# Kernel tuning notes

Measured on AMD Instinct MI355X. Metric: run time of the kernel, lower is better.

The kernel has to match this reference:

```python
import jax, jax.numpy as jnp
import numpy as np

BS, N_AGENTS, SA_DIM, HID = 2048, 64, 128, 256


def setup_inputs() -> dict:
    key = jax.random.key(0)
    ks = jax.random.split(key, 16)
    s = lambda fan_in: 1.0 / np.sqrt(fan_in)
    u = lambda k, shp, b: jax.random.uniform(k, shp, jnp.float32, -b, b)
    return {
        "x": jax.random.normal(ks[0], (BS, N_AGENTS, SA_DIM), jnp.float32),
        # encoder: Linear(sa, hid) -> Linear(hid, hid)
        "enc_w1": u(ks[1], (SA_DIM, HID), s(SA_DIM)),
        "enc_b1": u(ks[2], (HID,), s(SA_DIM)),
        "enc_w2": u(ks[3], (HID, HID), s(HID)),
        "enc_b2": u(ks[4], (HID,), s(HID)),
        # attention 'general' linear_in (no bias)
        "attn_w": u(ks[5], (HID, HID), s(HID)),
        # gc1: Linear(sa, hid); nn_gc1: Linear(sa, hid)
        "gc1_w": u(ks[6], (SA_DIM, HID), s(SA_DIM)),
        "gc1_b": u(ks[7], (HID,), s(SA_DIM)),
        "nn1_w": u(ks[8], (SA_DIM, HID), s(SA_DIM)),
        "nn1_b": u(ks[9], (HID,), s(SA_DIM)),
        # gc2: Linear(hid, hid); nn_gc2: Linear(hid, hid)
        "gc2_w": u(ks[10], (HID, HID), s(HID)),
        "gc2_b": u(ks[11], (HID,), s(HID)),
        "nn2_w": u(ks[12], (HID, HID), s(HID)),
        "nn2_b": u(ks[13], (HID,), s(HID)),
        "n_agents": N_AGENTS,
    }


def reference(x, enc_w1, enc_b1, enc_w2, enc_b2, attn_w,
              gc1_w, gc1_b, nn1_w, nn1_b, gc2_w, gc2_b, nn2_w, nn2_b,
              n_agents):
    relu = jax.nn.relu
    inv_n = 1.0 / n_agents
    # encoder MLP: relu(relu(x W1 + b1) W2 + b2)  -> [bs, n, hid]
    emb = relu(relu(x @ enc_w1 + enc_b1) @ enc_w2 + enc_b2)
    # general attention: softmax((emb W_a) emb^T) over last axis -> [bs, n, n]
    scores = jnp.einsum('bnd,bmd->bnm', emb @ attn_w, emb)
    attn = jax.nn.softmax(scores, axis=-1)
    # gc1: adj @ Linear(x); residual relu branch; normalize by n_agents
    feat = relu(jnp.einsum('bnm,bmh->bnh', attn, x @ gc1_w + gc1_b))
    feat = (feat + relu(x @ nn1_w + nn1_b)) * inv_n
    # gc2 on feat
    out = relu(jnp.einsum('bnm,bmh->bnh', attn, feat @ gc2_w + gc2_b))
    out = (out + relu(feat @ nn2_w + nn2_b)) * inv_n
    return out, attn
```

## Files before the change

### kernel.cpp

```cpp
#include <hip/hip_runtime.h>

typedef _Float16 half8 __attribute__((ext_vector_type(8)));
typedef _Float16 half4_t __attribute__((ext_vector_type(4)));
typedef float f32x4 __attribute__((ext_vector_type(4)));

#define NBATCH 2048
#define NA 64
#define SA 128
#define HID 256

#define OFF_R0 0
#define OFF_ATT 16384
#define SMEM_BYTES 40960

#define W_ENC1 0
#define W_ENC2 (W_ENC1 + 128 * 256)
#define W_ATTN (W_ENC2 + 256 * 256)
#define W_GC1 (W_ATTN + 256 * 256)
#define W_NN1 (W_GC1 + 128 * 256)
#define W_GC2 (W_NN1 + 128 * 256)
#define W_NN2 (W_GC2 + 256 * 256)

#define MFMA(a, b, cacc) __builtin_amdgcn_mfma_f32_16x16x32_f16((a), (b), (cacc), 0, 0, 0)

#define BAR()                                            \
  do {                                                   \
    asm volatile("s_waitcnt lgkmcnt(0)" ::: "memory");   \
    __builtin_amdgcn_s_barrier();                        \
  } while (0)

__global__ void pack_all(const float* __restrict__ e1, const float* __restrict__ e2,
                         const float* __restrict__ aw, const float* __restrict__ g1,
                         const float* __restrict__ n1, const float* __restrict__ g2,
                         const float* __restrict__ n2, _Float16* __restrict__ dst) {
  int b = (int)blockIdx.x;
  const float* src;
  int off;
  if (b < 16) { src = e1; off = W_ENC1; }
  else if (b < 48) { src = e2; off = W_ENC2; b -= 16; }
  else if (b < 80) { src = aw; off = W_ATTN; b -= 48; }
  else if (b < 96) { src = g1; off = W_GC1; b -= 80; }
  else if (b < 112) { src = n1; off = W_NN1; b -= 96; }
  else if (b < 144) { src = g2; off = W_GC2; b -= 112; }
  else { src = n2; off = W_NN2; b -= 144; }
  int t = b * 256 + (int)threadIdx.x;
  int lane = t & 63, frag = t >> 6;
  int nt = frag & 15, kt = frag >> 4;
  int g = lane >> 4, c = lane & 15;
  half8 h;
#pragma unroll
  for (int j = 0; j < 8; ++j)
    h[j] = (_Float16)src[(size_t)(kt * 32 + g * 8 + j) * 256 + nt * 16 + c];
  *(half8*)(dst + off + (size_t)t * 8) = h;
}

__global__ __launch_bounds__(256, 2) void dicg_main(
    const float* __restrict__ x, const float* __restrict__ b_enc1,
    const float* __restrict__ b_enc2, const float* __restrict__ b_gc1,
    const float* __restrict__ b_nn1, const float* __restrict__ b_gc2,
    const float* __restrict__ b_nn2, const _Float16* __restrict__ wp,
    float* __restrict__ out, float* __restrict__ attn_out) {
  extern __shared__ _Float16 sm[];
  _Float16* R0 = sm + OFF_R0;
  _Float16* ATTp = sm + OFF_ATT;

  const int tid = (int)threadIdx.x;
  const int wv = tid >> 6;
  const int lane = tid & 63;
  const int g = lane >> 4;
  const int c = lane & 15;
  const int bb = (int)blockIdx.x;
  const float* __restrict__ xb = x + (size_t)bb * (NA * SA);

  auto ldA = [&](const _Float16* p, int kt, int rt) -> half8 {
    return *(const half8*)(p + (kt * 4 + rt) * 512 + lane * 8);
  };
  auto ldB = [&](const _Float16* p, int kt, int ct) -> half8 {
    return *(const half8*)(p + (kt * 16 + ct) * 512 + lane * 8);
  };
  auto ldFeat = [&](int kt, int rt) -> half8 {
    return *(const half8*)(R0 + ((kt & 1) * 16 + 4 * (kt >> 1) + rt) * 512 + lane * 8);
  };
  auto wfrag = [&](const _Float16* wb, int kt, int ntg) -> half8 {
    return *(const half8*)(wb + ((size_t)(kt * 16 + ntg) * 64 + lane) * 8);
  };
  auto xfrag = [&](int r0, int k0) -> half8 {
    const float* p = xb + (r0 + c) * SA + k0 + g * 8;
    f32x4 u = *(const f32x4*)p;
    f32x4 v = *(const f32x4*)(p + 4);
    half8 h;
    h[0] = (_Float16)u[0]; h[1] = (_Float16)u[1];
    h[2] = (_Float16)u[2]; h[3] = (_Float16)u[3];
    h[4] = (_Float16)v[0]; h[5] = (_Float16)v[1];
    h[6] = (_Float16)v[2]; h[7] = (_Float16)v[3];
    return h;
  };

  auto stA_val = [&](_Float16* dst, int rt, int nt, int r, float v) {
    int kt = 2 * wv + (nt >> 1);
    int lanep = (2 * (nt & 1) + (c >> 3)) * 16 + 4 * g + r;
    dst[(kt * 4 + rt) * 512 + lanep * 8 + (c & 7)] = (_Float16)v;
  };
  auto ep_storeA = [&](f32x4(&acc)[4][4], const float* bias, bool dorelu) {
#pragma unroll
    for (int nt = 0; nt < 4; ++nt) {
      float bv = bias[64 * wv + 16 * nt + c];
#pragma unroll
      for (int rt = 0; rt < 4; ++rt)
#pragma unroll
        for (int r = 0; r < 4; ++r) {
          float y = acc[rt][nt][r] + bv;
          if (dorelu) y = fmaxf(y, 0.f);
          stA_val(R0, rt, nt, r, y);
        }
    }
  };
  auto ep_storeB = [&](f32x4(&acc)[4][4], const float* bias) {
#pragma unroll
    for (int nt = 0; nt < 4; ++nt) {
      float bv = bias[64 * wv + 16 * nt + c];
#pragma unroll
      for (int rt = 0; rt < 4; ++rt) {
        half4_t h;
#pragma unroll
        for (int r = 0; r < 4; ++r) h[r] = (_Float16)(acc[rt][nt][r] + bv);
        int fi = (rt >> 1) * 16 + 4 * wv + nt;
        int lanep = (2 * (rt & 1) + (g >> 1)) * 16 + c;
        *(half4_t*)(R0 + fi * 512 + lanep * 8 + 4 * (g & 1)) = h;
      }
    }
  };
  auto stFeatT = [&](int nt, int rt, half4_t hv) {
    int fi = (nt >> 1) * 16 + 4 * wv + rt;
    int lanep = (2 * (nt & 1) + (g >> 1)) * 16 + c;
    *(half4_t*)(R0 + fi * 512 + lanep * 8 + 4 * (g & 1)) = hv;
  };
  auto stQ = [&](const f32x4(&q2)[2], int s) {
    _Float16* base = ATTp + (wv + 4 * s) * 512;
#pragma unroll
    for (int nt2 = 0; nt2 < 2; ++nt2)
#pragma unroll
      for (int r = 0; r < 4; ++r)
        base[((2 * nt2 + (c >> 3)) * 16 + 4 * g + r) * 8 + (c & 7)] = (_Float16)q2[nt2][r];
  };

  half8 xr[4][4];
  half8 pf2[2][4];
  half8 pf7n[3][4], pf7g[3][4];

  {
    f32x4 acc[4][4]{};
#pragma unroll
    for (int kt = 0; kt < 4; ++kt) {
      half8 bf[4];
#pragma unroll
      for (int rt = 0; rt < 4; ++rt) xr[kt][rt] = xfrag(16 * rt, kt * 32);
#pragma unroll
      for (int nt = 0; nt < 4; ++nt) bf[nt] = wfrag(wp + W_ENC1, kt, 4 * wv + nt);
#pragma unroll
      for (int rt = 0; rt < 4; ++rt)
#pragma unroll
        for (int nt = 0; nt < 4; ++nt) acc[rt][nt] = MFMA(xr[kt][rt], bf[nt], acc[rt][nt]);
    }
#pragma unroll
    for (int s = 0; s < 2; ++s)
#pragma unroll
      for (int nt = 0; nt < 4; ++nt) pf2[s][nt] = wfrag(wp + W_ENC2, s, 4 * wv + nt);
    ep_storeA(acc, b_enc1, true);
  }
  BAR();
  {
    f32x4 acc[4][4]{};
#pragma unroll
    for (int kt = 0; kt < 8; ++kt) {
      half8 af[4], bf[4];
#pragma unroll
      for (int rt = 0; rt < 4; ++rt) af[rt] = ldA(R0, kt, rt);
#pragma unroll
      for (int nt = 0; nt < 4; ++nt)
        bf[nt] = (kt < 2) ? pf2[kt][nt] : wfrag(wp + W_ENC2, kt, 4 * wv + nt);
#pragma unroll
      for (int rt = 0; rt < 4; ++rt)
#pragma unroll
        for (int nt = 0; nt < 4; ++nt) acc[rt][nt] = MFMA(af[rt], bf[nt], acc[rt][nt]);
    }
    BAR();
    ep_storeA(acc, b_enc2, true);
  }
  BAR();
  {
    half8 aeK[8];
#pragma unroll
    for (int k2 = 0; k2 < 8; ++k2) aeK[k2] = ldA(R0, k2, wv);
    f32x4 sc[4]{};
    {
      f32x4 q2[2]{};
#pragma unroll
      for (int k2 = 0; k2 < 8; ++k2) {
        q2[0] = MFMA(aeK[k2], wfrag(wp + W_ATTN, k2, 0), q2[0]);
        q2[1] = MFMA(aeK[k2], wfrag(wp + W_ATTN, k2, 1), q2[1]);
      }
      stQ(q2, 0);
    }
#pragma unroll
    for (int ktp = 0; ktp < 8; ++ktp) {
      f32x4 q2n[2]{};
      if (ktp < 7) {
#pragma unroll
        for (int k2 = 0; k2 < 8; ++k2) {
          q2n[0] = MFMA(aeK[k2], wfrag(wp + W_ATTN, k2, 2 * ktp + 2), q2n[0]);
          q2n[1] = MFMA(aeK[k2], wfrag(wp + W_ATTN, k2, 2 * ktp + 3), q2n[1]);
        }
      }
      asm volatile("s_waitcnt lgkmcnt(0)" ::: "memory");
      half8 qb = *(const half8*)(ATTp + (wv + 4 * (ktp & 1)) * 512 + lane * 8);
      if (ktp < 7) stQ(q2n, (ktp + 1) & 1);
#pragma unroll
      for (int rt = 0; rt < 4; ++rt) sc[rt] = MFMA(ldA(R0, ktp, rt), qb, sc[rt]);
    }
    float m = sc[0][0];
#pragma unroll
    for (int rt = 0; rt < 4; ++rt)
#pragma unroll
      for (int r = 0; r < 4; ++r) m = fmaxf(m, sc[rt][r]);
    m = fmaxf(m, __shfl_xor(m, 16));
    m = fmaxf(m, __shfl_xor(m, 32));
    float e[4][4], s = 0.f;
#pragma unroll
    for (int rt = 0; rt < 4; ++rt)
#pragma unroll
      for (int r = 0; r < 4; ++r) {
        e[rt][r] = __expf(sc[rt][r] - m);
        s += e[rt][r];
      }
    s += __shfl_xor(s, 16);
    s += __shfl_xor(s, 32);
    float inv = 1.0f / s;
    float* ao = attn_out + ((size_t)bb * NA + 16 * wv + c) * NA;
#pragma unroll
    for (int rt = 0; rt < 4; ++rt) {
      f32x4 vv;
      half4_t hh;
#pragma unroll
      for (int r = 0; r < 4; ++r) {
        vv[r] = e[rt][r] * inv;
        hh[r] = (_Float16)vv[r];
      }
      *(f32x4*)(ao + 16 * rt + 4 * g) = vv;
      int fi = (rt >> 1) * 4 + wv;
      int lanep = (2 * (rt & 1) + (g >> 1)) * 16 + c;
      *(half4_t*)(ATTp + fi * 512 + lanep * 8 + 4 * (g & 1)) = hh;
    }
  }
  BAR();
  half4_t r1h[4][4];
  {
    f32x4 aG[4][4]{}, aN[4][4]{};
#pragma unroll
    for (int kt = 0; kt < 4; ++kt) {
      half8 b1[4], b2[4];
#pragma unroll
      for (int nt = 0; nt < 4; ++nt) b1[nt] = wfrag(wp + W_GC1, kt, 4 * wv + nt);
#pragma unroll
      for (int nt = 0; nt < 4; ++nt) b2[nt] = wfrag(wp + W_NN1, kt, 4 * wv + nt);
#pragma unroll
      for (int rt = 0; rt < 4; ++rt)
#pragma unroll
        for (int nt = 0; nt < 4; ++nt) {
          aG[rt][nt] = MFMA(xr[kt][rt], b1[nt], aG[rt][nt]);
          aN[nt][rt] = MFMA(b2[nt], xr[kt][rt], aN[nt][rt]);
        }
    }
    ep_storeB(aG, b_gc1);
#pragma unroll
    for (int nt = 0; nt < 4; ++nt) {
      f32x4 bv4 = *(const f32x4*)(b_nn1 + 64 * wv + 16 * nt + 4 * g);
#pragma unroll
      for (int rt = 0; rt < 4; ++rt)
#pragma unroll
        for (int r = 0; r < 4; ++r)
          r1h[nt][rt][r] = (_Float16)fmaxf(aN[nt][rt][r] + bv4[r], 0.f);
    }
#pragma unroll
    for (int s2 = 0; s2 < 2; ++s2)
#pragma unroll
      for (int nt = 0; nt < 4; ++nt) {
        pf7n[s2][nt] = wfrag(wp + W_NN2, s2, 4 * wv + nt);
        pf7g[s2][nt] = wfrag(wp + W_GC2, s2, 4 * wv + nt);
      }
  }
  {
#pragma unroll
    for (int nt = 0; nt < 4; ++nt) {
      pf7n[2][nt] = wfrag(wp + W_NN2, 2, 4 * wv + nt);
      pf7g[2][nt] = wfrag(wp + W_GC2, 2, 4 * wv + nt);
    }
    f32x4 a1[4][4]{};
#pragma unroll
    for (int kt = 0; kt < 2; ++kt) {
      half8 af[4], bf[4];
#pragma unroll
      for (int rt = 0; rt < 4; ++rt) af[rt] = ldA(ATTp, kt, rt);
#pragma unroll
      for (int nt = 0; nt < 4; ++nt) bf[nt] = ldB(R0, kt, 4 * wv + nt);
#pragma unroll
      for (int rt = 0; rt < 4; ++rt)
#pragma unroll
        for (int nt = 0; nt < 4; ++nt) a1[nt][rt] = MFMA(bf[nt], af[rt], a1[nt][rt]);
    }
#pragma unroll
    for (int nt = 0; nt < 4; ++nt)
#pragma unroll
      for (int rt = 0; rt < 4; ++rt) {
        half4_t hv;
#pragma unroll
        for (int r = 0; r < 4; ++r)
          hv[r] = (_Float16)((fmaxf(a1[nt][rt][r], 0.f) + (float)r1h[nt][rt][r]) *
                             0.015625f);
        stFeatT(nt, rt, hv);
      }
  }
  BAR();
  half4_t r2h[4][4];
  {
    f32x4 aN2[4][4]{}, aG2[4][4]{};
#pragma unroll
    for (int kt = 0; kt < 8; ++kt) {
      half8 af[4], b1[4], b2[4];
#pragma unroll
      for (int rt = 0; rt < 4; ++rt) af[rt] = ldFeat(kt, rt);
#pragma unroll
      for (int nt = 0; nt < 4; ++nt)
        b1[nt] = (kt < 3) ? pf7n[kt][nt] : wfrag(wp + W_NN2, kt, 4 * wv + nt);
#pragma unroll
      for (int nt = 0; nt < 4; ++nt)
        b2[nt] = (kt < 3) ? pf7g[kt][nt] : wfrag(wp + W_GC2, kt, 4 * wv + nt);
#pragma unroll
      for (int rt = 0; rt < 4; ++rt)
#pragma unroll
        for (int nt = 0; nt < 4; ++nt) {
          aN2[nt][rt] = MFMA(b1[nt], af[rt], aN2[nt][rt]);
          aG2[rt][nt] = MFMA(af[rt], b2[nt], aG2[rt][nt]);
        }
    }
#pragma unroll
    for (int nt = 0; nt < 4; ++nt) {
      f32x4 bv4 = *(const f32x4*)(b_nn2 + 64 * wv + 16 * nt + 4 * g);
#pragma unroll
      for (int rt = 0; rt < 4; ++rt)
#pragma unroll
        for (int r = 0; r < 4; ++r)
          r2h[nt][rt][r] = (_Float16)fmaxf(aN2[nt][rt][r] + bv4[r], 0.f);
    }
    BAR();
    ep_storeB(aG2, b_gc2);
  }
  {
    f32x4 a1[4][4]{};
#pragma unroll
    for (int kt = 0; kt < 2; ++kt) {
      half8 af[4], bf[4];
#pragma unroll
      for (int rt = 0; rt < 4; ++rt) af[rt] = ldA(ATTp, kt, rt);
#pragma unroll
      for (int nt = 0; nt < 4; ++nt) bf[nt] = ldB(R0, kt, 4 * wv + nt);
#pragma unroll
      for (int rt = 0; rt < 4; ++rt)
#pragma unroll
        for (int nt = 0; nt < 4; ++nt) a1[nt][rt] = MFMA(bf[nt], af[rt], a1[nt][rt]);
    }
    float* ob = out + (size_t)bb * NA * HID;
#pragma unroll
    for (int nt = 0; nt < 4; ++nt)
#pragma unroll
      for (int rt = 0; rt < 4; ++rt) {
        f32x4 vv;
#pragma unroll
        for (int r = 0; r < 4; ++r)
          vv[r] = (fmaxf(a1[nt][rt][r], 0.f) + (float)r2h[nt][rt][r]) * 0.015625f;
        *(f32x4*)(ob + (size_t)(16 * rt + c) * HID + 64 * wv + 16 * nt + 4 * g) = vv;
      }
  }
}

extern "C" void kernel_launch(void* const* d_in, const int* in_sizes, int n_in,
                              void* d_out, int out_size, void* d_ws, size_t ws_size,
                              hipStream_t stream) {
  const float* x = (const float*)d_in[0];
  const float* enc_w1 = (const float*)d_in[1];
  const float* enc_b1 = (const float*)d_in[2];
  const float* enc_w2 = (const float*)d_in[3];
  const float* enc_b2 = (const float*)d_in[4];
  const float* attn_w = (const float*)d_in[5];
  const float* gc1_w = (const float*)d_in[6];
  const float* gc1_b = (const float*)d_in[7];
  const float* nn1_w = (const float*)d_in[8];
  const float* nn1_b = (const float*)d_in[9];
  const float* gc2_w = (const float*)d_in[10];
  const float* gc2_b = (const float*)d_in[11];
  const float* nn2_w = (const float*)d_in[12];
  const float* nn2_b = (const float*)d_in[13];

  _Float16* wp = (_Float16*)d_ws;
  float* out = (float*)d_out;
  float* attn_o = out + (size_t)NBATCH * NA * HID;

  pack_all<<<176, 256, 0, stream>>>(enc_w1, enc_w2, attn_w, gc1_w, nn1_w, gc2_w,
                                    nn2_w, wp);
  dicg_main<<<NBATCH, 256, SMEM_BYTES, stream>>>(
      x, enc_b1, enc_b2, gc1_b, nn1_b, gc2_b, nn2_b, wp, out, attn_o);
}
```

Baseline: 159.7 us.

## Cut register pressure to fit three blocks per CU via chunked GEMMs

Raises the launch-bounds minimum from two to three blocks per multiprocessor. To fit the smaller per-thread register budget, it drops the cached x fragments (reloading them from global memory in the gc1/nn1 stage), halves the accumulator tiles by splitting the gc1/nn1 and gc2/nn2 GEMMs into two column chunks, and shrinks the prefetched weight fragments. This trades extra global reloads of x and weights, plus less instruction-level overlap, for higher occupancy and better latency hiding. The gc2 output is now kept in fp16 registers and written to shared memory after the barrier.

```diff
diff --git a/kernel.cpp b/kernel.cpp
--- a/kernel.cpp
+++ b/kernel.cpp
@@ -54,7 +54,7 @@
   *(half8*)(dst + off + (size_t)t * 8) = h;
 }
 
-__global__ __launch_bounds__(256, 2) void dicg_main(
+__global__ __launch_bounds__(256, 3) void dicg_main(
     const float* __restrict__ x, const float* __restrict__ b_enc1,
     const float* __restrict__ b_enc2, const float* __restrict__ b_gc1,
     const float* __restrict__ b_nn1, const float* __restrict__ b_gc2,
@@ -115,20 +115,10 @@
         }
     }
   };
-  auto ep_storeB = [&](f32x4(&acc)[4][4], const float* bias) {
-#pragma unroll
-    for (int nt = 0; nt < 4; ++nt) {
-      float bv = bias[64 * wv + 16 * nt + c];
-#pragma unroll
-      for (int rt = 0; rt < 4; ++rt) {
-        half4_t h;
-#pragma unroll
-        for (int r = 0; r < 4; ++r) h[r] = (_Float16)(acc[rt][nt][r] + bv);
-        int fi = (rt >> 1) * 16 + 4 * wv + nt;
-        int lanep = (2 * (rt & 1) + (g >> 1)) * 16 + c;
-        *(half4_t*)(R0 + fi * 512 + lanep * 8 + 4 * (g & 1)) = h;
-      }
-    }
+  auto stB4 = [&](int rt, int ntg, half4_t h) {
+    int fi = (rt >> 1) * 16 + 4 * wv + ntg;
+    int lanep = (2 * (rt & 1) + (g >> 1)) * 16 + c;
+    *(half4_t*)(R0 + fi * 512 + lanep * 8 + 4 * (g & 1)) = h;
   };
   auto stFeatT = [&](int nt, int rt, half4_t hv) {
     int fi = (nt >> 1) * 16 + 4 * wv + rt;
@@ -144,23 +134,22 @@
         base[((2 * nt2 + (c >> 3)) * 16 + 4 * g + r) * 8 + (c & 7)] = (_Float16)q2[nt2][r];
   };
 
-  half8 xr[4][4];
   half8 pf2[2][4];
-  half8 pf7n[3][4], pf7g[3][4];
+  half8 pf7n[4], pf7g[4];
 
   {
     f32x4 acc[4][4]{};
 #pragma unroll
     for (int kt = 0; kt < 4; ++kt) {
-      half8 bf[4];
-#pragma unroll
-      for (int rt = 0; rt < 4; ++rt) xr[kt][rt] = xfrag(16 * rt, kt * 32);
+      half8 af[4], bf[4];
+#pragma unroll
+      for (int rt = 0; rt < 4; ++rt) af[rt] = xfrag(16 * rt, kt * 32);
 #pragma unroll
       for (int nt = 0; nt < 4; ++nt) bf[nt] = wfrag(wp + W_ENC1, kt, 4 * wv + nt);
 #pragma unroll
       for (int rt = 0; rt < 4; ++rt)
 #pragma unroll
-        for (int nt = 0; nt < 4; ++nt) acc[rt][nt] = MFMA(xr[kt][rt], bf[nt], acc[rt][nt]);
+        for (int nt = 0; nt < 4; ++nt) acc[rt][nt] = MFMA(af[rt], bf[nt], acc[rt][nt]);
     }
 #pragma unroll
     for (int s = 0; s < 2; ++s)
@@ -254,46 +243,51 @@
   }
   BAR();
   half4_t r1h[4][4];
+#pragma unroll
+  for (int ch = 0; ch < 2; ++ch) {
+    f32x4 aG[4][2]{}, aN[2][4]{};
+#pragma unroll
+    for (int kt = 0; kt < 4; ++kt) {
+      half8 af[4], b1[2], b2[2];
+#pragma unroll
+      for (int rt = 0; rt < 4; ++rt) af[rt] = xfrag(16 * rt, kt * 32);
+#pragma unroll
+      for (int ntl = 0; ntl < 2; ++ntl) {
+        b1[ntl] = wfrag(wp + W_GC1, kt, 4 * wv + 2 * ch + ntl);
+        b2[ntl] = wfrag(wp + W_NN1, kt, 4 * wv + 2 * ch + ntl);
+      }
+#pragma unroll
+      for (int rt = 0; rt < 4; ++rt)
+#pragma unroll
+        for (int ntl = 0; ntl < 2; ++ntl) {
+          aG[rt][ntl] = MFMA(af[rt], b1[ntl], aG[rt][ntl]);
+          aN[ntl][rt] = MFMA(b2[ntl], af[rt], aN[ntl][rt]);
+        }
+    }
+#pragma unroll
+    for (int ntl = 0; ntl < 2; ++ntl) {
+      int ntg = 2 * ch + ntl;
+      float bvg = b_gc1[64 * wv + 16 * ntg + c];
+#pragma unroll
+      for (int rt = 0; rt < 4; ++rt) {
+        half4_t h;
+#pragma unroll
+        for (int r = 0; r < 4; ++r) h[r] = (_Float16)(aG[rt][ntl][r] + bvg);
+        stB4(rt, ntg, h);
+      }
+      f32x4 bv4 = *(const f32x4*)(b_nn1 + 64 * wv + 16 * ntg + 4 * g);
+#pragma unroll
+      for (int rt = 0; rt < 4; ++rt)
+#pragma unroll
+        for (int r = 0; r < 4; ++r)
+          r1h[ntg][rt][r] = (_Float16)fmaxf(aN[ntl][rt][r] + bv4[r], 0.f);
+    }
+  }
   {
-    f32x4 aG[4][4]{}, aN[4][4]{};
-#pragma unroll
-    for (int kt = 0; kt < 4; ++kt) {
-      half8 b1[4], b2[4];
-#pragma unroll
-      for (int nt = 0; nt < 4; ++nt) b1[nt] = wfrag(wp + W_GC1, kt, 4 * wv + nt);
-#pragma unroll
-      for (int nt = 0; nt < 4; ++nt) b2[nt] = wfrag(wp + W_NN1, kt, 4 * wv + nt);
-#pragma unroll
-      for (int rt = 0; rt < 4; ++rt)
-#pragma unroll
-        for (int nt = 0; nt < 4; ++nt) {
-          aG[rt][nt] = MFMA(xr[kt][rt], b1[nt], aG[rt][nt]);
-          aN[nt][rt] = MFMA(b2[nt], xr[kt][rt], aN[nt][rt]);
-        }
-    }
-    ep_storeB(aG, b_gc1);
 #pragma unroll
     for (int nt = 0; nt < 4; ++nt) {
-      f32x4 bv4 = *(const f32x4*)(b_nn1 + 64 * wv + 16 * nt + 4 * g);
-#pragma unroll
-      for (int rt = 0; rt < 4; ++rt)
-#pragma unroll
-        for (int r = 0; r < 4; ++r)
-          r1h[nt][rt][r] = (_Float16)fmaxf(aN[nt][rt][r] + bv4[r], 0.f);
-    }
-#pragma unroll
-    for (int s2 = 0; s2 < 2; ++s2)
-#pragma unroll
-      for (int nt = 0; nt < 4; ++nt) {
-        pf7n[s2][nt] = wfrag(wp + W_NN2, s2, 4 * wv + nt);
-        pf7g[s2][nt] = wfrag(wp + W_GC2, s2, 4 * wv + nt);
-      }
-  }
-  {
-#pragma unroll
-    for (int nt = 0; nt < 4; ++nt) {
-      pf7n[2][nt] = wfrag(wp + W_NN2, 2, 4 * wv + nt);
-      pf7g[2][nt] = wfrag(wp + W_GC2, 2, 4 * wv + nt);
+      pf7n[nt] = wfrag(wp + W_NN2, 0, 4 * wv + nt);
+      pf7g[nt] = wfrag(wp + W_GC2, 0, 4 * wv + nt);
     }
     f32x4 a1[4][4]{};
 #pragma unroll
@@ -322,39 +316,51 @@
   }
   BAR();
   half4_t r2h[4][4];
-  {
-    f32x4 aN2[4][4]{}, aG2[4][4]{};
+  half4_t g2h[4][4];
+#pragma unroll
+  for (int ch = 0; ch < 2; ++ch) {
+    f32x4 aN2[2][4]{}, aG2[4][2]{};
 #pragma unroll
     for (int kt = 0; kt < 8; ++kt) {
-      half8 af[4], b1[4], b2[4];
+      half8 af[4], b1[2], b2[2];
 #pragma unroll
       for (int rt = 0; rt < 4; ++rt) af[rt] = ldFeat(kt, rt);
 #pragma unroll
-      for (int nt = 0; nt < 4; ++nt)
-        b1[nt] = (kt < 3) ? pf7n[kt][nt] : wfrag(wp + W_NN2, kt, 4 * wv + nt);
-#pragma unroll
-      for (int nt = 0; nt < 4; ++nt)
-        b2[nt] = (kt < 3) ? pf7g[kt][nt] : wfrag(wp + W_GC2, kt, 4 * wv + nt);
-#pragma unroll
-      for (int rt = 0; rt < 4; ++rt)
-#pragma unroll
-        for (int nt = 0; nt < 4; ++nt) {
-          aN2[nt][rt] = MFMA(b1[nt], af[rt], aN2[nt][rt]);
-          aG2[rt][nt] = MFMA(af[rt], b2[nt], aG2[rt][nt]);
+      for (int ntl = 0; ntl < 2; ++ntl) {
+        int ntg = 2 * ch + ntl;
+        b1[ntl] = (kt == 0) ? pf7n[ntg] : wfrag(wp + W_NN2, kt, 4 * wv + ntg);
+        b2[ntl] = (kt == 0) ? pf7g[ntg] : wfrag(wp + W_GC2, kt, 4 * wv + ntg);
+      }
+#pragma unroll
+      for (int rt = 0; rt < 4; ++rt)
+#pragma unroll
+        for (int ntl = 0; ntl < 2; ++ntl) {
+          aN2[ntl][rt] = MFMA(b1[ntl], af[rt], aN2[ntl][rt]);
+          aG2[rt][ntl] = MFMA(af[rt], b2[ntl], aG2[rt][ntl]);
         }
     }
 #pragma unroll
-    for (int nt = 0; nt < 4; ++nt) {
-      f32x4 bv4 = *(const f32x4*)(b_nn2 + 64 * wv + 16 * nt + 4 * g);
+    for (int ntl = 0; ntl < 2; ++ntl) {
+      int ntg = 2 * ch + ntl;
+      f32x4 bv4 = *(const f32x4*)(b_nn2 + 64 * wv + 16 * ntg + 4 * g);
 #pragma unroll
       for (int rt = 0; rt < 4; ++rt)
 #pragma unroll
         for (int r = 0; r < 4; ++r)
-          r2h[nt][rt][r] = (_Float16)fmaxf(aN2[nt][rt][r] + bv4[r], 0.f);
-    }
-    BAR();
-    ep_storeB(aG2, b_gc2);
-  }
+          r2h[ntg][rt][r] = (_Float16)fmaxf(aN2[ntl][rt][r] + bv4[r], 0.f);
+      float bvg = b_gc2[64 * wv + 16 * ntg + c];
+#pragma unroll
+      for (int rt = 0; rt < 4; ++rt)
+#pragma unroll
+        for (int r = 0; r < 4; ++r)
+          g2h[ntg][rt][r] = (_Float16)(aG2[rt][ntl][r] + bvg);
+    }
+  }
+  BAR();
+#pragma unroll
+  for (int ntg = 0; ntg < 4; ++ntg)
+#pragma unroll
+    for (int rt = 0; rt < 4; ++rt) stB4(rt, ntg, g2h[ntg][rt]);
   {
     f32x4 a1[4][4]{};
 #pragma unroll
```

Result: slower. 314.0 us (+96.7%).
